# Kernel tuning notes

Hardware: AMD Instinct MI355X
Metric: run time of the kernel (lower is better)

The kernel has to match this reference:

```python
import jax, jax.numpy as jnp
import numpy as np

D_MODEL = 512
H = 8
DK = D_MODEL // H  # 64


def setup_inputs() -> dict:
    key = jax.random.key(0)
    ks = jax.random.split(key, 8)
    B, S = 2, 4096
    q = jax.random.normal(ks[0], (B, S, D_MODEL), dtype=jnp.float32)
    k = jax.random.normal(ks[1], (B, S, D_MODEL), dtype=jnp.float32)
    v = jax.random.normal(ks[2], (B, S, D_MODEL), dtype=jnp.float32)
    # per-head projection weights, torch nn.Linear layout [out, in], stacked over heads
    scale = 1.0 / np.sqrt(D_MODEL)
    Wq = jax.random.uniform(ks[3], (H, DK, D_MODEL), jnp.float32, -scale, scale)
    Wk = jax.random.uniform(ks[4], (H, DK, D_MODEL), jnp.float32, -scale, scale)
    Wv = jax.random.uniform(ks[5], (H, DK, D_MODEL), jnp.float32, -scale, scale)
    Wo = jax.random.uniform(ks[6], (D_MODEL, D_MODEL), jnp.float32, -scale, scale)
    # causal mask (True = keep), matches masked_fill(mask.logical_not(), -inf)
    mask = jnp.tril(jnp.ones((S, S), dtype=jnp.bool_))
    return {"q": q, "k": k, "v": v, "Wq": Wq, "Wk": Wk, "Wv": Wv, "Wo": Wo, "mask": mask}


def reference(q, k, v, Wq, Wk, Wv, Wo, mask):
    # per-head projections (stacked): x @ W^T for each head -> [B, H, S, DK]
    qh = jnp.einsum('bsd,hed->bhse', q, Wq)
    kh = jnp.einsum('bsd,hed->bhse', k, Wk)
    vh = jnp.einsum('bsd,hed->bhse', v, Wv)
    scaling = 1.0 / np.sqrt(DK)
    scores = jnp.einsum('bhse,bhte->bhst', qh, kh) * scaling  # [B,H,S,S]
    scores = jnp.where(mask, scores, -jnp.inf)
    attn = jax.nn.softmax(scores, axis=-1)
    heads = jnp.einsum('bhst,bhte->bhse', attn, vh)  # [B,H,S,DK]
    B, _, S, _ = heads.shape
    concat = jnp.transpose(heads, (0, 2, 1, 3)).reshape(B, S, D_MODEL)
    return concat @ Wo.T
```

## Files before the change

### kernel.cpp

```cpp
#include <hip/hip_runtime.h>
#include <hip/hip_bf16.h>
#include <math.h>

typedef __bf16 bf16_t;
typedef __bf16 bf16x8 __attribute__((ext_vector_type(8)));
typedef __bf16 bf16x4 __attribute__((ext_vector_type(4)));
typedef short short4v __attribute__((ext_vector_type(4)));
typedef float f32x4 __attribute__((ext_vector_type(4)));

__device__ __forceinline__ f32x4 mfma_k32(bf16x8 a, bf16x8 b, f32x4 c) {
    return __builtin_amdgcn_mfma_f32_16x16x32_bf16(a, b, c, 0, 0, 0);
}

__device__ __forceinline__ f32x4 mfma_k16(bf16x4 a, bf16x4 b, f32x4 c) {
#if __has_builtin(__builtin_amdgcn_mfma_f32_16x16x16_bf16)
    return __builtin_amdgcn_mfma_f32_16x16x16_bf16(a, b, c, 0, 0, 0);
#elif __has_builtin(__builtin_amdgcn_mfma_f32_16x16x16bf16_1k)
    short4v as, bs;
    __builtin_memcpy(&as, &a, 8);
    __builtin_memcpy(&bs, &b, 8);
    return __builtin_amdgcn_mfma_f32_16x16x16bf16_1k(as, bs, c, 0, 0, 0);
#else
    f32x4 d = c;
    asm volatile("v_mfma_f32_16x16x16_bf16 %0, %1, %2, %0" : "+v"(d) : "v"(a), "v"(b));
    return d;
#endif
}

__device__ __forceinline__ float fast_exp2(float x) {
#if __has_builtin(__builtin_amdgcn_exp2f)
    return __builtin_amdgcn_exp2f(x);
#else
    float r;
    asm("v_exp_f32 %0, %1" : "=v"(r) : "v"(x));
    return r;
#endif
}

__device__ __forceinline__ void async16(const bf16_t* g, __bf16* l) {
    __builtin_amdgcn_global_load_lds(
        (const __attribute__((address_space(1))) void*)g,
        (__attribute__((address_space(3))) void*)l, 16, 0, 0);
}

__device__ __forceinline__ int swz_col(int col, int row) {
    return (col & ~63) | ((((col >> 3) & 7) ^ (row & 7)) << 3) | (col & 7);
}

__global__ __launch_bounds__(256) void cvt_all(const float* __restrict__ q,
                                               const float* __restrict__ k,
                                               const float* __restrict__ v,
                                               const float* __restrict__ Wq,
                                               const float* __restrict__ Wk,
                                               const float* __restrict__ Wv,
                                               const float* __restrict__ Wo,
                                               bf16_t* __restrict__ qc,
                                               bf16_t* __restrict__ kc,
                                               bf16_t* __restrict__ vc,
                                               bf16_t* __restrict__ Wc) {
    const int bx = blockIdx.x;
    if (bx < 2048) {
        size_t i = ((size_t)bx * 256 + threadIdx.x) * 8;
        int row = (int)(i >> 9), col = (int)(i & 511);
        size_t di = (size_t)row * 512 + swz_col(col, row);
        float4 a0 = *(const float4*)(q + i), a1 = *(const float4*)(q + i + 4);
        float4 b0 = *(const float4*)(k + i), b1 = *(const float4*)(k + i + 4);
        float4 c0 = *(const float4*)(v + i), c1 = *(const float4*)(v + i + 4);
        bf16x8 qo, ko, vo;
        qo[0]=(__bf16)a0.x; qo[1]=(__bf16)a0.y; qo[2]=(__bf16)a0.z; qo[3]=(__bf16)a0.w;
        qo[4]=(__bf16)a1.x; qo[5]=(__bf16)a1.y; qo[6]=(__bf16)a1.z; qo[7]=(__bf16)a1.w;
        ko[0]=(__bf16)b0.x; ko[1]=(__bf16)b0.y; ko[2]=(__bf16)b0.z; ko[3]=(__bf16)b0.w;
        ko[4]=(__bf16)b1.x; ko[5]=(__bf16)b1.y; ko[6]=(__bf16)b1.z; ko[7]=(__bf16)b1.w;
        vo[0]=(__bf16)c0.x; vo[1]=(__bf16)c0.y; vo[2]=(__bf16)c0.z; vo[3]=(__bf16)c0.w;
        vo[4]=(__bf16)c1.x; vo[5]=(__bf16)c1.y; vo[6]=(__bf16)c1.z; vo[7]=(__bf16)c1.w;
        *(bf16x8*)(qc + di) = qo;
        *(bf16x8*)(kc + di) = ko;
        *(bf16x8*)(vc + di) = vo;
    } else {
        const int b2 = bx - 2048;
        const int m = b2 >> 7;
        const float* src = m == 0 ? Wq : m == 1 ? Wk : m == 2 ? Wv : Wo;
        const float sc = (m == 0) ? 0.125f * 1.44269504088896f : 1.0f;
        size_t i = ((size_t)(b2 & 127) * 256 + threadIdx.x) * 8;
        int row = (int)(i >> 9), col = (int)(i & 511);
        float4 a0 = *(const float4*)(src + i), a1 = *(const float4*)(src + i + 4);
        bf16x8 o;
        o[0]=(__bf16)(a0.x*sc); o[1]=(__bf16)(a0.y*sc); o[2]=(__bf16)(a0.z*sc); o[3]=(__bf16)(a0.w*sc);
        o[4]=(__bf16)(a1.x*sc); o[5]=(__bf16)(a1.y*sc); o[6]=(__bf16)(a1.z*sc); o[7]=(__bf16)(a1.w*sc);
        *(bf16x8*)(Wc + (size_t)m * 262144 + (size_t)row * 512 + swz_col(col, row)) = o;
    }
}

__global__ __launch_bounds__(256) void proj_fused(const bf16_t* __restrict__ xs,
                                                  const bf16_t* __restrict__ Wc,
                                                  bf16_t* __restrict__ qh,
                                                  bf16_t* __restrict__ kh,
                                                  bf16_t* __restrict__ vh) {
    __shared__ __bf16 Asm[16 * 64];
    __shared__ __bf16 Bsm[512 * 64];
    const int z    = blockIdx.z;
    const bf16_t* A = xs + (size_t)z * 4194304;
    const bf16_t* B = Wc + (size_t)z * 262144;
    const int tid  = threadIdx.x;
    const int wave = tid >> 6;
    const int lane = tid & 63;
    const int quad = lane >> 4;
    const int l16  = lane & 15;
    const int swz  = l16 & 7;
    const int m0 = blockIdx.x * 16;
    const int r8 = lane >> 3;
    const int c8 = (lane & 7) * 8;

    f32x4 acc[8];
    for (int i = 0; i < 8; ++i) acc[i] = (f32x4){0.f, 0.f, 0.f, 0.f};

    for (int kt = 0; kt < 512; kt += 64) {
        __syncthreads();
        if (wave < 2)
            async16(A + (size_t)(m0 + wave * 8 + r8) * 512 + kt + c8, &Asm[wave * 8 * 64]);
        for (int j = 0; j < 16; ++j)
            async16(B + (size_t)(wave * 128 + j * 8 + r8) * 512 + kt + c8,
                    &Bsm[(wave * 128 + j * 8) * 64]);
        __syncthreads();

        for (int ks = 0; ks < 2; ++ks) {
            bf16x8 afr = *(const bf16x8*)&Asm[l16 * 64 + ((ks * 4 + quad) ^ swz) * 8];
            for (int nt = 0; nt < 8; ++nt) {
                bf16x8 bfr = *(const bf16x8*)&Bsm[(wave * 128 + nt * 16 + l16) * 64 + ((ks * 4 + quad) ^ swz) * 8];
                acc[nt] = mfma_k32(afr, bfr, acc[nt]);
            }
        }
    }

    if (z < 2) {
        bf16_t* out = z ? kh : qh;
        for (int nt = 0; nt < 8; ++nt) {
            int e = wave * 128 + nt * 16 + l16;
            int h = e >> 6, el = e & 63;
            for (int r = 0; r < 4; ++r) {
                int row = m0 + quad * 4 + r;
                int b = row >> 12, s = row & 4095;
                int elp = (((el >> 3) ^ (row & 7)) << 3) | (el & 7);
                out[(((size_t)(b * 8 + h)) * 4096 + s) * 64 + elp] = (bf16_t)acc[nt][r];
            }
        }
    } else {
        const int bb = m0 >> 12;
        const int sbase = (m0 & 4095) & ~63;
        const int s5 = (m0 >> 5) & 1;
        const int mf4 = ((m0 >> 4) & 1) * 4;
        const int chunk = 2 * quad + s5;
        for (int nt = 0; nt < 8; ++nt) {
            int e_g = wave * 128 + nt * 16 + l16;
            int h = e_g >> 6, el = e_g & 63;
            int col = sbase + ((chunk ^ (e_g & 7)) << 3) + mf4;
            bf16x4 pk;
            pk[0] = (bf16_t)acc[nt][0]; pk[1] = (bf16_t)acc[nt][1];
            pk[2] = (bf16_t)acc[nt][2]; pk[3] = (bf16_t)acc[nt][3];
            *(bf16x4*)&vh[(((size_t)(bb * 8 + h)) * 64 + el) * 4096 + col] = pk;
        }
    }
}

__global__ __launch_bounds__(256) void gemm_final(const bf16_t* __restrict__ A,
                                                  const bf16_t* __restrict__ B,
                                                  float* __restrict__ out) {
    __shared__ __bf16 Asm[16 * 64];
    __shared__ __bf16 Bsm[512 * 64];
    const int tid  = threadIdx.x;
    const int wave = tid >> 6;
    const int lane = tid & 63;
    const int quad = lane >> 4;
    const int l16  = lane & 15;
    const int swz  = l16 & 7;
    const int m0 = blockIdx.x * 16;
    const int r8 = lane >> 3;
    const int c8 = (lane & 7) * 8;

    f32x4 acc[8];
    for (int i = 0; i < 8; ++i) acc[i] = (f32x4){0.f, 0.f, 0.f, 0.f};

    for (int kt = 0; kt < 512; kt += 64) {
        __syncthreads();
        if (wave < 2)
            async16(A + (size_t)(m0 + wave * 8 + r8) * 512 + kt + c8, &Asm[wave * 8 * 64]);
        for (int j = 0; j < 16; ++j)
            async16(B + (size_t)(wave * 128 + j * 8 + r8) * 512 + kt + c8,
                    &Bsm[(wave * 128 + j * 8) * 64]);
        __syncthreads();

        for (int ks = 0; ks < 2; ++ks) {
            bf16x8 afr = *(const bf16x8*)&Asm[l16 * 64 + ((ks * 4 + quad) ^ swz) * 8];
            for (int nt = 0; nt < 8; ++nt) {
                bf16x8 bfr = *(const bf16x8*)&Bsm[(wave * 128 + nt * 16 + l16) * 64 + ((ks * 4 + quad) ^ swz) * 8];
                acc[nt] = mfma_k32(afr, bfr, acc[nt]);
            }
        }
    }

    for (int nt = 0; nt < 8; ++nt) {
        int n = wave * 128 + nt * 16 + l16;
        for (int r = 0; r < 4; ++r)
            out[(size_t)(m0 + quad * 4 + r) * 512 + n] = acc[nt][r];
    }
}

__global__ __launch_bounds__(512, 4) void attn_kernel(const bf16_t* __restrict__ qh,
                                                      const bf16_t* __restrict__ kh,
                                                      const bf16_t* __restrict__ vh,
                                                      bf16_t* __restrict__ ao) {
    __shared__ __bf16 SM[32768];
    __bf16* KSM = &SM[0];
    __bf16* VSM = &SM[16384];
    float* Osc = (float*)SM;
    float* Lsc = (float*)&SM[24576];

    const int tid  = threadIdx.x;
    const int wave = tid >> 6;
    const int pp   = wave >> 1;
    const int wl   = wave & 1;
    const int lane = tid & 63;
    const int quad = lane >> 4;
    const int l16  = lane & 15;
    const int swz  = l16 & 7;
    const int bh   = blockIdx.y;
    const size_t base = (size_t)bh * 4096 * 64;
    const int r8 = lane >> 3;
    const int c8 = (lane & 7) * 8;
    const int b = bh >> 3, h = bh & 7;

    for (int leg = 0; leg < 2; ++leg) {
        const int qt = leg ? (63 - (int)blockIdx.x) : (int)blockIdx.x;
        const int q0 = qt * 64;

        bf16x8 qf[2][2];
        for (int g = 0; g < 2; ++g) {
            const bf16_t* qp = qh + base + (size_t)(q0 + wl * 32 + g * 16 + l16) * 64;
            qf[g][0] = *(const bf16x8*)(qp + ((quad ^ swz) * 8));
            qf[g][1] = *(const bf16x8*)(qp + (((4 + quad) ^ swz) * 8));
        }

        f32x4 o[2][4];
        for (int g = 0; g < 2; ++g)
            for (int i = 0; i < 4; ++i) o[g][i] = (f32x4){0.f, 0.f, 0.f, 0.f};
        float lsum[2] = {0.f, 0.f};

        const int iters = (qt + 4) >> 2;
        for (int it = 0; it < iters; ++it) {
            const int j0 = it * 256;
            const int koff = j0 + pp * 64 - q0;
            __syncthreads();
            if (koff <= 63) {
                for (int j = 0; j < 4; ++j) {
                    int row = wl * 32 + j * 8 + r8;
                    async16(kh + base + (size_t)(j0 + pp * 64 + row) * 64 + c8,
                            KSM + (pp * 64 + wl * 32 + j * 8) * 64);
                    async16(vh + (size_t)(bh * 64 + row) * 4096 + j0 + pp * 64 + c8,
                            VSM + (pp * 64 + wl * 32 + j * 8) * 64);
                }
            }
            __syncthreads();
            if (koff > wl * 32 + 31) continue;

            f32x4 st[2][4];
            for (int nt = 0; nt < 4; ++nt) {
                const __bf16* kr = KSM + (pp * 64 + nt * 16 + l16) * 64;
                bf16x8 kf0 = *(const bf16x8*)(kr + ((quad ^ swz) * 8));
                bf16x8 kf1 = *(const bf16x8*)(kr + (((4 + quad) ^ swz) * 8));
                for (int g = 0; g < 2; ++g) {
                    f32x4 zz = (f32x4){0.f, 0.f, 0.f, 0.f};
                    zz = mfma_k32(kf0, qf[g][0], zz);
                    zz = mfma_k32(kf1, qf[g][1], zz);
                    st[g][nt] = zz;
                }
            }

            bf16x4 pf[2][4];
            for (int g = 0; g < 2; ++g) {
                const int qb = wl * 32 + g * 16;
                if (koff + 63 <= qb) {
                    for (int nt = 0; nt < 4; ++nt)
                        for (int r = 0; r < 4; ++r) {
                            float p = fast_exp2(st[g][nt][r]);
                            lsum[g] += p;
                            pf[g][nt][r] = (bf16_t)p;
                        }
                } else {
                    const int qrow = qb + l16;
                    for (int nt = 0; nt < 4; ++nt)
                        for (int r = 0; r < 4; ++r) {
                            int key = nt * 16 + quad * 4 + r;
                            float p = (key + koff <= qrow) ? fast_exp2(st[g][nt][r]) : 0.f;
                            lsum[g] += p;
                            pf[g][nt][r] = (bf16_t)p;
                        }
                }
            }

            for (int dt = 0; dt < 4; ++dt)
                for (int kt2 = 0; kt2 < 2; ++kt2) {
                    bf16x8 vf = *(const bf16x8*)&VSM[(pp * 64 + dt * 16 + l16) * 64 + (((2 * quad + kt2) ^ swz) * 8)];
                    bf16x4 vlo = {vf[0], vf[1], vf[2], vf[3]};
                    bf16x4 vhi = {vf[4], vf[5], vf[6], vf[7]};
                    for (int g = 0; g < 2; ++g) {
                        o[g][dt] = mfma_k16(pf[g][2 * kt2], vlo, o[g][dt]);
                        o[g][dt] = mfma_k16(pf[g][2 * kt2 + 1], vhi, o[g][dt]);
                    }
                }
        }

        __syncthreads();
        if (pp != 0) {
            const int pi = pp - 1;
            for (int g = 0; g < 2; ++g) {
                float ls = lsum[g];
                ls += __shfl_xor(ls, 16);
                ls += __shfl_xor(ls, 32);
                const int qb = (pi * 2 + wl) * 32 + g * 16;
                Lsc[qb + l16] = ls;
                for (int dt = 0; dt < 4; ++dt)
                    for (int r = 0; r < 4; ++r)
                        Osc[(qb + quad * 4 + r) * 64 + dt * 16 + l16] = o[g][dt][r];
            }
        }
        __syncthreads();
        if (pp == 0) {
            for (int g = 0; g < 2; ++g) {
                float ls = lsum[g];
                ls += __shfl_xor(ls, 16);
                ls += __shfl_xor(ls, 32);
                const int qb = wl * 32 + g * 16;
                for (int pi = 0; pi < 3; ++pi)
                    ls += Lsc[(pi * 2 + wl) * 32 + g * 16 + l16];
                float linv[4];
                for (int r = 0; r < 4; ++r) linv[r] = 1.0f / __shfl(ls, quad * 4 + r);
                for (int r = 0; r < 4; ++r) {
                    int s_g = q0 + qb + quad * 4 + r;
                    size_t rowoff = ((size_t)(b * 4096 + s_g)) * 512;
                    for (int dt = 0; dt < 4; ++dt) {
                        float ov = o[g][dt][r];
                        for (int pi = 0; pi < 3; ++pi)
                            ov += Osc[((pi * 2 + wl) * 32 + g * 16 + quad * 4 + r) * 64 + dt * 16 + l16];
                        int el = dt * 16 + l16;
                        int elp = (((el >> 3) ^ (s_g & 7)) << 3) | (el & 7);
                        ao[rowoff + h * 64 + elp] = (bf16_t)(ov * linv[r]);
                    }
                }
            }
        }
    }
}

extern "C" void kernel_launch(void* const* d_in, const int* in_sizes, int n_in,
                              void* d_out, int out_size, void* d_ws, size_t ws_size,
                              hipStream_t stream) {
    const float* q  = (const float*)d_in[0];
    const float* k  = (const float*)d_in[1];
    const float* v  = (const float*)d_in[2];
    const float* Wq = (const float*)d_in[3];
    const float* Wk = (const float*)d_in[4];
    const float* Wv = (const float*)d_in[5];
    const float* Wo = (const float*)d_in[6];
    float* out = (float*)d_out;

    bf16_t* ws = (bf16_t*)d_ws;
    const size_t R = (size_t)8192 * 512;
    bf16_t* qc = ws;
    bf16_t* kc = ws + R;
    bf16_t* vc = ws + 2 * R;
    bf16_t* vh = ws + 3 * R;
    bf16_t* Wc = ws + 4 * R;
    bf16_t* qh = (bf16_t*)d_out;
    bf16_t* kh = (bf16_t*)d_out + R;
    bf16_t* ao = qc;

    cvt_all<<<dim3(2560), dim3(256), 0, stream>>>(q, k, v, Wq, Wk, Wv, Wo, qc, kc, vc, Wc);
    proj_fused<<<dim3(512, 1, 3), dim3(256), 0, stream>>>(ws, Wc, qh, kh, vh);
    attn_kernel<<<dim3(32, 16), dim3(512), 0, stream>>>(qh, kh, vh, ao);
    gemm_final<<<dim3(512), dim3(256), 0, stream>>>(ao, Wc + 3 * 262144, out);
}
```

Before: 285.8 us.

## Retile projection and output GEMMs to square 128x128 block tiles

```diff
diff --git a/kernel.cpp b/kernel.cpp
--- a/kernel.cpp
+++ b/kernel.cpp
@@ -91,118 +91,111 @@
     }
 }
 
-__global__ __launch_bounds__(256) void proj_fused(const bf16_t* __restrict__ xs,
-                                                  const bf16_t* __restrict__ Wc,
-                                                  bf16_t* __restrict__ qh,
-                                                  bf16_t* __restrict__ kh,
-                                                  bf16_t* __restrict__ vh) {
-    __shared__ __bf16 Asm[16 * 64];
-    __shared__ __bf16 Bsm[512 * 64];
-    const int z    = blockIdx.z;
-    const bf16_t* A = xs + (size_t)z * 4194304;
-    const bf16_t* B = Wc + (size_t)z * 262144;
+template<int MODE>
+__device__ __forceinline__ void gemm128_body(const bf16_t* __restrict__ A,
+                                             const bf16_t* __restrict__ B,
+                                             void* __restrict__ outp,
+                                             int m0, int n0) {
+    __shared__ __bf16 Asm[128 * 64];
+    __shared__ __bf16 Bsm[128 * 64];
     const int tid  = threadIdx.x;
     const int wave = tid >> 6;
     const int lane = tid & 63;
     const int quad = lane >> 4;
     const int l16  = lane & 15;
     const int swz  = l16 & 7;
-    const int m0 = blockIdx.x * 16;
     const int r8 = lane >> 3;
     const int c8 = (lane & 7) * 8;
-
-    f32x4 acc[8];
-    for (int i = 0; i < 8; ++i) acc[i] = (f32x4){0.f, 0.f, 0.f, 0.f};
+    const int mrow0 = (wave & 1) * 64;
+    const int ncol0 = (wave >> 1) * 64;
+
+    f32x4 acc[4][4];
+    for (int i = 0; i < 4; ++i)
+        for (int j = 0; j < 4; ++j) acc[i][j] = (f32x4){0.f, 0.f, 0.f, 0.f};
 
     for (int kt = 0; kt < 512; kt += 64) {
         __syncthreads();
-        if (wave < 2)
-            async16(A + (size_t)(m0 + wave * 8 + r8) * 512 + kt + c8, &Asm[wave * 8 * 64]);
-        for (int j = 0; j < 16; ++j)
-            async16(B + (size_t)(wave * 128 + j * 8 + r8) * 512 + kt + c8,
-                    &Bsm[(wave * 128 + j * 8) * 64]);
+        for (int j = 0; j < 4; ++j) {
+            async16(A + (size_t)(m0 + wave * 32 + j * 8 + r8) * 512 + kt + c8,
+                    &Asm[(wave * 32 + j * 8) * 64]);
+            async16(B + (size_t)(n0 + wave * 32 + j * 8 + r8) * 512 + kt + c8,
+                    &Bsm[(wave * 32 + j * 8) * 64]);
+        }
         __syncthreads();
 
         for (int ks = 0; ks < 2; ++ks) {
-            bf16x8 afr = *(const bf16x8*)&Asm[l16 * 64 + ((ks * 4 + quad) ^ swz) * 8];
-            for (int nt = 0; nt < 8; ++nt) {
-                bf16x8 bfr = *(const bf16x8*)&Bsm[(wave * 128 + nt * 16 + l16) * 64 + ((ks * 4 + quad) ^ swz) * 8];
-                acc[nt] = mfma_k32(afr, bfr, acc[nt]);
+            bf16x8 af[4];
+            for (int mt = 0; mt < 4; ++mt)
+                af[mt] = *(const bf16x8*)&Asm[(mrow0 + mt * 16 + l16) * 64 + ((ks * 4 + quad) ^ swz) * 8];
+            for (int nt = 0; nt < 4; ++nt) {
+                bf16x8 bf = *(const bf16x8*)&Bsm[(ncol0 + nt * 16 + l16) * 64 + ((ks * 4 + quad) ^ swz) * 8];
+                for (int mt = 0; mt < 4; ++mt)
+                    acc[mt][nt] = mfma_k32(af[mt], bf, acc[mt][nt]);
             }
         }
     }
 
-    if (z < 2) {
-        bf16_t* out = z ? kh : qh;
-        for (int nt = 0; nt < 8; ++nt) {
-            int e = wave * 128 + nt * 16 + l16;
+    if (MODE == 0) {
+        bf16_t* out = (bf16_t*)outp;
+        for (int nt = 0; nt < 4; ++nt) {
+            int e = n0 + ncol0 + nt * 16 + l16;
             int h = e >> 6, el = e & 63;
-            for (int r = 0; r < 4; ++r) {
-                int row = m0 + quad * 4 + r;
-                int b = row >> 12, s = row & 4095;
-                int elp = (((el >> 3) ^ (row & 7)) << 3) | (el & 7);
-                out[(((size_t)(b * 8 + h)) * 4096 + s) * 64 + elp] = (bf16_t)acc[nt][r];
-            }
+            for (int mt = 0; mt < 4; ++mt)
+                for (int r = 0; r < 4; ++r) {
+                    int row = m0 + mrow0 + mt * 16 + quad * 4 + r;
+                    int b = row >> 12, s = row & 4095;
+                    int elp = (((el >> 3) ^ (row & 7)) << 3) | (el & 7);
+                    out[(((size_t)(b * 8 + h)) * 4096 + s) * 64 + elp] = (bf16_t)acc[mt][nt][r];
+                }
+        }
+    } else if (MODE == 1) {
+        bf16_t* out = (bf16_t*)outp;
+        for (int nt = 0; nt < 4; ++nt) {
+            int s_g = n0 + ncol0 + nt * 16 + l16;
+            int b = s_g >> 12;
+            int sbase = (s_g & 4095) & ~63;
+            int f = 16 * ((l16 >> 2) & 3) + 4 * nt + (l16 & 3);
+            for (int mt = 0; mt < 4; ++mt)
+                for (int r = 0; r < 4; ++r) {
+                    int e_g = m0 + mrow0 + mt * 16 + quad * 4 + r;
+                    int h = e_g >> 6, el = e_g & 63;
+                    int col = sbase | ((((f >> 3) ^ (e_g & 7)) & 7) << 3) | (f & 7);
+                    out[(((size_t)(b * 8 + h)) * 64 + el) * 4096 + col] = (bf16_t)acc[mt][nt][r];
+                }
         }
     } else {
-        const int bb = m0 >> 12;
-        const int sbase = (m0 & 4095) & ~63;
-        const int s5 = (m0 >> 5) & 1;
-        const int mf4 = ((m0 >> 4) & 1) * 4;
-        const int chunk = 2 * quad + s5;
-        for (int nt = 0; nt < 8; ++nt) {
-            int e_g = wave * 128 + nt * 16 + l16;
-            int h = e_g >> 6, el = e_g & 63;
-            int col = sbase + ((chunk ^ (e_g & 7)) << 3) + mf4;
-            bf16x4 pk;
-            pk[0] = (bf16_t)acc[nt][0]; pk[1] = (bf16_t)acc[nt][1];
-            pk[2] = (bf16_t)acc[nt][2]; pk[3] = (bf16_t)acc[nt][3];
-            *(bf16x4*)&vh[(((size_t)(bb * 8 + h)) * 64 + el) * 4096 + col] = pk;
+        float* out = (float*)outp;
+        for (int nt = 0; nt < 4; ++nt) {
+            int n = n0 + ncol0 + nt * 16 + l16;
+            for (int mt = 0; mt < 4; ++mt)
+                for (int r = 0; r < 4; ++r) {
+                    int row = m0 + mrow0 + mt * 16 + quad * 4 + r;
+                    out[(size_t)row * 512 + n] = acc[mt][nt][r];
+                }
         }
     }
+}
+
+__global__ __launch_bounds__(256) void proj_fused(const bf16_t* __restrict__ xs,
+                                                  const bf16_t* __restrict__ Wc,
+                                                  bf16_t* __restrict__ qh,
+                                                  bf16_t* __restrict__ kh,
+                                                  bf16_t* __restrict__ vh) {
+    const int z = blockIdx.z;
+    const bf16_t* X = xs + (size_t)z * 4194304;
+    const bf16_t* W = Wc + (size_t)z * 262144;
+    if (z == 0)
+        gemm128_body<0>(X, W, qh, blockIdx.x * 128, blockIdx.y * 128);
+    else if (z == 1)
+        gemm128_body<0>(X, W, kh, blockIdx.x * 128, blockIdx.y * 128);
+    else
+        gemm128_body<1>(W, X, vh, blockIdx.y * 128, blockIdx.x * 128);
 }
 
 __global__ __launch_bounds__(256) void gemm_final(const bf16_t* __restrict__ A,
                                                   const bf16_t* __restrict__ B,
                                                   float* __restrict__ out) {
-    __shared__ __bf16 Asm[16 * 64];
-    __shared__ __bf16 Bsm[512 * 64];
-    const int tid  = threadIdx.x;
-    const int wave = tid >> 6;
-    const int lane = tid & 63;
-    const int quad = lane >> 4;
-    const int l16  = lane & 15;
-    const int swz  = l16 & 7;
-    const int m0 = blockIdx.x * 16;
-    const int r8 = lane >> 3;
-    const int c8 = (lane & 7) * 8;
-
-    f32x4 acc[8];
-    for (int i = 0; i < 8; ++i) acc[i] = (f32x4){0.f, 0.f, 0.f, 0.f};
-
-    for (int kt = 0; kt < 512; kt += 64) {
-        __syncthreads();
-        if (wave < 2)
-            async16(A + (size_t)(m0 + wave * 8 + r8) * 512 + kt + c8, &Asm[wave * 8 * 64]);
-        for (int j = 0; j < 16; ++j)
-            async16(B + (size_t)(wave * 128 + j * 8 + r8) * 512 + kt + c8,
-                    &Bsm[(wave * 128 + j * 8) * 64]);
-        __syncthreads();
-
-        for (int ks = 0; ks < 2; ++ks) {
-            bf16x8 afr = *(const bf16x8*)&Asm[l16 * 64 + ((ks * 4 + quad) ^ swz) * 8];
-            for (int nt = 0; nt < 8; ++nt) {
-                bf16x8 bfr = *(const bf16x8*)&Bsm[(wave * 128 + nt * 16 + l16) * 64 + ((ks * 4 + quad) ^ swz) * 8];
-                acc[nt] = mfma_k32(afr, bfr, acc[nt]);
-            }
-        }
-    }
-
-    for (int nt = 0; nt < 8; ++nt) {
-        int n = wave * 128 + nt * 16 + l16;
-        for (int r = 0; r < 4; ++r)
-            out[(size_t)(m0 + quad * 4 + r) * 512 + n] = acc[nt][r];
-    }
+    gemm128_body<2>(A, B, out, blockIdx.x * 128, blockIdx.y * 128);
 }
 
 __global__ __launch_bounds__(512, 4) void attn_kernel(const bf16_t* __restrict__ qh,
@@ -375,7 +368,7 @@
     bf16_t* ao = qc;
 
     cvt_all<<<dim3(2560), dim3(256), 0, stream>>>(q, k, v, Wq, Wk, Wv, Wo, qc, kc, vc, Wc);
-    proj_fused<<<dim3(512, 1, 3), dim3(256), 0, stream>>>(ws, Wc, qh, kh, vh);
+    proj_fused<<<dim3(64, 4, 3), dim3(256), 0, stream>>>(ws, Wc, qh, kh, vh);
     attn_kernel<<<dim3(32, 16), dim3(512), 0, stream>>>(qh, kh, vh, ao);
-    gemm_final<<<dim3(512), dim3(256), 0, stream>>>(ao, Wc + 3 * 262144, out);
-}
+    gemm_final<<<dim3(64, 4), dim3(256), 0, stream>>>(ao, Wc + 3 * 262144, out);
+}
```

After: 264.2 us. -7.6%, faster.
